# Performance work log

Hardware: AMD Instinct MI355X
Metric: run time of the kernel (lower is better)

Reference implementation:

```python
import jax, jax.numpy as jnp
import numpy as np

N_ACTIVE = 200000
K = 9  # filter_size [1,3,3] -> 9 kernel offsets
C = 64
EPS = 1e-5

def setup_inputs() -> dict:
    key = jax.random.key(0)
    ks = jax.random.split(key, 4)
    features = jax.random.normal(ks[0], (N_ACTIVE, C), dtype=jnp.float32)
    # rulebook: neighbor index per (active site, kernel offset); N_ACTIVE is the
    # sentinel meaning 'no active neighbor at this offset'
    nbr = jax.random.randint(ks[1], (N_ACTIVE, K), 0, N_ACTIVE + 1, dtype=jnp.int32)
    # identity offset (center of 3x3) always maps to self, as in submanifold conv
    nbr = nbr.at[:, K // 2].set(jnp.arange(N_ACTIVE, dtype=jnp.int32))
    W1 = jax.random.normal(ks[2], (K, C, C), dtype=jnp.float32) * (2.0 / (K * C)) ** 0.5
    W2 = jax.random.normal(ks[3], (K, C, C), dtype=jnp.float32) * (2.0 / (K * C)) ** 0.5
    gamma1 = jnp.ones((C,), jnp.float32); beta1 = jnp.zeros((C,), jnp.float32)
    gamma2 = jnp.ones((C,), jnp.float32); beta2 = jnp.zeros((C,), jnp.float32)
    return {"features": features, "nbr": nbr, "W1": W1, "gamma1": gamma1,
            "beta1": beta1, "W2": W2, "gamma2": gamma2, "beta2": beta2}

def _subm_conv(x, nbr, W):
    # gather-GEMM(-scatter) submanifold conv over active voxels
    xp = jnp.concatenate([x, jnp.zeros((1, x.shape[1]), x.dtype)], axis=0)  # zero row for sentinel
    g = xp[nbr]  # [N, K, Cin] irregular gather
    return jnp.einsum('nkc,kcd->nd', g, W)

def _bn(x, gamma, beta):
    mu = jnp.mean(x, axis=0)
    var = jnp.var(x, axis=0)
    return (x - mu) * jax.lax.rsqrt(var + EPS) * gamma + beta

def reference(features, nbr, W1, gamma1, beta1, W2, gamma2, beta2):
    out = _subm_conv(features, nbr, W1)
    out = jax.nn.relu(_bn(out, gamma1, beta1))   # scn.BatchNormReLU
    out = _subm_conv(out, nbr, W2)
    out = _bn(out, gamma2, beta2)                # scn.BatchNormalization
    return out + features                        # scn.AddTable with Identity residual
```

## Files before the change

### kernel.cpp

```cpp
#include <hip/hip_runtime.h>
#include <hip/hip_bf16.h>

#define NS 200000
#define KF 9
#define CC 64
#define RPB 128
#define NB ((NS + RPB - 1) / RPB)

typedef __bf16 bf16_t;
typedef __bf16 bf16x8 __attribute__((ext_vector_type(8)));
typedef __bf16 bf16x4 __attribute__((ext_vector_type(4)));
typedef float f32x4 __attribute__((ext_vector_type(4)));

__global__ void k_prep(const float* __restrict__ x, const float* __restrict__ W1,
                       const float* __restrict__ W2, bf16_t* __restrict__ xb,
                       bf16_t* __restrict__ W1p, bf16_t* __restrict__ W2p,
                       float* __restrict__ stats , float* __restrict__ zrow ) {
  const int b = blockIdx.x;
  const int tid = threadIdx.x;
  if (b < 12500) {
    if (b == 0) {
      stats[tid] = 0.f;
      if (tid < 32) zrow[tid] = 0.f;
    }
    long base = ((long)b * 256 + tid) * 4;
    const float4 v = *(const float4*)(x + base);
    bf16x4 o;
    o[0] = (bf16_t)v.x; o[1] = (bf16_t)v.y; o[2] = (bf16_t)v.z; o[3] = (bf16_t)v.w;
    *(bf16x4*)(xb + base) = o;
    return;
  }
  int b2 = b - 12500;
  const float* W = (b2 < 144) ? W1 : W2;
  bf16_t* Wp = (b2 < 144) ? W1p : W2p;
  if (b2 >= 144) b2 -= 144;
  int p = b2 * 256 + tid;
  int j = p & 7;
  int lane = (p >> 3) & 63;
  int kstep = (p >> 9) & 1;
  int ntile = (p >> 10) & 3;
  int k = p >> 12;
  int col = ntile * 16 + (lane & 15);
  int kk = kstep * 32 + 8 * (lane >> 4) + j;
  Wp[p] = (bf16_t)W[(k * CC + kk) * CC + col];
}

template <int OUT_F32>
__global__ __launch_bounds__(256, 3) void k_conv(
    const bf16_t* __restrict__ xb,
    const int* __restrict__ nbr,
    const bf16_t* __restrict__ Wp,
    void* __restrict__ yv,
    float* __restrict__ stats,
    const char* __restrict__ zrow)
{
  __shared__ int nbr_s[RPB * KF];
  __shared__ float lred[8 * CC];

  const int tid = threadIdx.x;
  const int lane = tid & 63;
  const int wid = tid >> 6;
  const int row0 = blockIdx.x * RPB;
  const int l15 = lane & 15;
  const int lhi = lane >> 4;

  {
    const long nbase = (long)row0 * KF;
    const long ntot = (long)NS * KF;
#pragma unroll
    for (int t = 0; t < 5; ++t) {
      int p = tid + t * 256;
      if (p < RPB * KF) {
        long g = nbase + p;
        nbr_s[p] = (g < ntot) ? nbr[g] : NS;
      }
    }
  }
  __syncthreads();

  const char* xbb = (const char*)xb;
  const bf16x8* wp = (const bf16x8*)Wp;
  const int r_lo = (32 * wid + l15) * KF;
  const int r_hi = (32 * wid + 16 + l15) * KF;

  auto rowptr = [&](int u) -> const char* {
    return ((unsigned)u < NS) ? (xbb + (size_t)(unsigned)u * 128u) : zrow;
  };

  int id0[KF], id1[KF];
#pragma unroll
  for (int k = 0; k < KF; ++k) { id0[k] = nbr_s[r_lo + k]; id1[k] = nbr_s[r_hi + k]; }

  f32x4 acc[2][4];
#pragma unroll
  for (int m = 0; m < 2; ++m)
#pragma unroll
    for (int n = 0; n < 4; ++n) acc[m][n] = (f32x4){0.f, 0.f, 0.f, 0.f};

  bf16x8 Af[4][2][2];
  bf16x8 cB[4][2], nB[4][2];

  auto loadA = [&](int slot, int k) {
    const char* s0 = rowptr(id0[k]);
    const char* s1 = rowptr(id1[k]);
    Af[slot][0][0] = *(const bf16x8*)(s0 + lhi * 16);
    Af[slot][0][1] = *(const bf16x8*)(s0 + 64 + lhi * 16);
    Af[slot][1][0] = *(const bf16x8*)(s1 + lhi * 16);
    Af[slot][1][1] = *(const bf16x8*)(s1 + 64 + lhi * 16);
  };

#pragma unroll
  for (int n = 0; n < 4; ++n)
#pragma unroll
    for (int kk = 0; kk < 2; ++kk)
      cB[n][kk] = wp[((0 * 4 + n) * 2 + kk) * 64 + lane];
#pragma unroll
  for (int k = 0; k < 3; ++k) loadA(k, k);

#pragma unroll
  for (int k = 0; k < KF; ++k) {
    if (k + 3 < KF) loadA((k + 3) & 3, k + 3);
    if (k + 1 < KF) {
#pragma unroll
      for (int n = 0; n < 4; ++n)
#pragma unroll
        for (int kk = 0; kk < 2; ++kk)
          nB[n][kk] = wp[(((k + 1) * 4 + n) * 2 + kk) * 64 + lane];
    }
    const int sl = k & 3;
    __builtin_amdgcn_s_setprio(1);
#pragma unroll
    for (int m = 0; m < 2; ++m)
#pragma unroll
      for (int n = 0; n < 4; ++n)
        acc[m][n] = __builtin_amdgcn_mfma_f32_16x16x32_bf16(Af[sl][m][0], cB[n][0], acc[m][n], 0, 0, 0);
#pragma unroll
    for (int m = 0; m < 2; ++m)
#pragma unroll
      for (int n = 0; n < 4; ++n)
        acc[m][n] = __builtin_amdgcn_mfma_f32_16x16x32_bf16(Af[sl][m][1], cB[n][1], acc[m][n], 0, 0, 0);
    __builtin_amdgcn_s_setprio(0);
#pragma unroll
    for (int n = 0; n < 4; ++n) { cB[n][0] = nB[n][0]; cB[n][1] = nB[n][1]; }
  }

  float csum[4] = {0.f, 0.f, 0.f, 0.f}, csq[4] = {0.f, 0.f, 0.f, 0.f};
  bf16_t* yb = (bf16_t*)yv;
  float* yf = (float*)yv;
#pragma unroll
  for (int m = 0; m < 2; ++m) {
    const int rb0 = row0 + 32 * wid + 16 * m + 4 * lhi;
#pragma unroll
    for (int n = 0; n < 4; ++n) {
      const int col = 16 * n + l15;
#pragma unroll
      for (int j = 0; j < 4; ++j) {
        float v = acc[m][n][j];
        csum[n] += v; csq[n] += v * v;
        int rb = rb0 + j;
        if (rb < NS) {
          if (OUT_F32) yf[(long)rb * CC + col] = v;
          else         yb[(long)rb * CC + col] = (bf16_t)v;
        }
      }
    }
  }
#pragma unroll
  for (int n = 0; n < 4; ++n) {
    csum[n] += __shfl_xor(csum[n], 16); csum[n] += __shfl_xor(csum[n], 32);
    csq[n]  += __shfl_xor(csq[n], 16);  csq[n]  += __shfl_xor(csq[n], 32);
  }
  if (lane < 16) {
#pragma unroll
    for (int n = 0; n < 4; ++n) {
      lred[wid * CC + 16 * n + l15] = csum[n];
      lred[4 * CC + wid * CC + 16 * n + l15] = csq[n];
    }
  }
  __syncthreads();
  if (tid < CC) {
    float s = lred[tid] + lred[CC + tid] + lred[2 * CC + tid] + lred[3 * CC + tid];
    float q = lred[4 * CC + tid] + lred[5 * CC + tid] + lred[6 * CC + tid] + lred[7 * CC + tid];
    atomicAdd(&stats[tid], s);
    atomicAdd(&stats[64 + tid], q);
  }
}

__global__ void k_bnrelu(const bf16_t* __restrict__ in, const float* __restrict__ stats,
                         const float* __restrict__ gamma, const float* __restrict__ beta,
                         bf16_t* __restrict__ out) {
  __shared__ float ss_s[128];
  const int tid = threadIdx.x;
  if (tid < 64) {
    const float invN = 1.0f / (float)NS;
    float mean = stats[tid] * invN;
    float var = fmaxf(stats[64 + tid] * invN - mean * mean, 0.f);
    float rs = rsqrtf(var + 1e-5f);
    float sc = gamma[tid] * rs;
    ss_s[tid] = sc;
    ss_s[64 + tid] = beta[tid] - mean * sc;
  }
  __syncthreads();
  long base = ((long)blockIdx.x * 256 + tid) * 8;
  bf16x8 v = *(const bf16x8*)(in + base);
  int c0 = (int)(base & 63);
  bf16x8 o;
#pragma unroll
  for (int j = 0; j < 8; ++j) {
    float f = (float)v[j] * ss_s[c0 + j] + ss_s[64 + c0 + j];
    o[j] = (bf16_t)fmaxf(f, 0.f);
  }
  *(bf16x8*)(out + base) = o;
}

__global__ void k_final(float* __restrict__ io, const float* __restrict__ stats,
                        const float* __restrict__ gamma, const float* __restrict__ beta,
                        const float* __restrict__ x) {
  __shared__ float ss_s[128];
  const int tid = threadIdx.x;
  if (tid < 64) {
    const float invN = 1.0f / (float)NS;
    float mean = stats[tid] * invN;
    float var = fmaxf(stats[64 + tid] * invN - mean * mean, 0.f);
    float rs = rsqrtf(var + 1e-5f);
    float sc = gamma[tid] * rs;
    ss_s[tid] = sc;
    ss_s[64 + tid] = beta[tid] - mean * sc;
  }
  __syncthreads();
  long base = ((long)blockIdx.x * 256 + tid) * 4;
  float4 v = *(const float4*)(io + base);
  float4 f = *(const float4*)(x + base);
  int c0 = (int)(base & 63);
  v.x = v.x * ss_s[c0 + 0] + ss_s[64 + c0 + 0] + f.x;
  v.y = v.y * ss_s[c0 + 1] + ss_s[64 + c0 + 1] + f.y;
  v.z = v.z * ss_s[c0 + 2] + ss_s[64 + c0 + 2] + f.z;
  v.w = v.w * ss_s[c0 + 3] + ss_s[64 + c0 + 3] + f.w;
  *(float4*)(io + base) = v;
}

extern "C" void kernel_launch(void* const* d_in, const int* in_sizes, int n_in,
                              void* d_out, int out_size, void* d_ws, size_t ws_size,
                              hipStream_t stream) {
  const float* features = (const float*)d_in[0];
  const int* nbr        = (const int*)d_in[1];
  const float* W1       = (const float*)d_in[2];
  const float* gamma1   = (const float*)d_in[3];
  const float* beta1    = (const float*)d_in[4];
  const float* W2       = (const float*)d_in[5];
  const float* gamma2   = (const float*)d_in[6];
  const float* beta2    = (const float*)d_in[7];

  bf16_t* xb  = (bf16_t*)d_out;
  bf16_t* o1  = (bf16_t*)((char*)d_out + (size_t)NS * CC * 2);
  float*  o2f = (float*)d_out;

  char* ws = (char*)d_ws;
  auto alignup = [](size_t x) { return (x + 255) & ~(size_t)255; };
  size_t off = 0;
  bf16_t* y1n = (bf16_t*)(ws + off); off += alignup((size_t)NS * CC * 2);
  bf16_t* W1p = (bf16_t*)(ws + off); off += alignup((size_t)KF * 4096 * 2);
  bf16_t* W2p = (bf16_t*)(ws + off); off += alignup((size_t)KF * 4096 * 2);
  float* stats = (float*)(ws + off); off += alignup(256 * 4);
  float* zrow  = (float*)(ws + off); off += alignup(32 * 4);

  k_prep<<<12500 + 288, 256, 0, stream>>>(features, W1, W2, xb, W1p, W2p, stats, zrow);

  k_conv<0><<<NB, 256, 0, stream>>>(xb, nbr, W1p, (void*)o1, stats, (const char*)zrow);
  k_bnrelu<<<6250, 256, 0, stream>>>(o1, stats, gamma1, beta1, y1n);

  k_conv<1><<<NB, 256, 0, stream>>>(y1n, nbr, W2p, (void*)o2f, stats + 128, (const char*)zrow);
  k_final<<<12500, 256, 0, stream>>>(o2f, stats + 128, gamma2, beta2, features);
}
```

Baseline: 283.7 us.

## Fuse BN+ReLU into second conv gather and stage rows via LDS async loads

Removes the separate BN-ReLU pass by applying the scale, shift and ReLU to gathered neighbor rows inside the second conv, masking the shift for sentinel rows. Gathered rows now go through a swizzled three-slot LDS ring using global_load_lds with explicit vmcnt waits, instead of being loaded straight into registers. Rows per block drop to 64, with one MFMA row tile per wave and an occupancy hint of 4. The second conv writes bf16 and the final kernel reads it, which cuts intermediate traffic at some precision cost. The scale and shift are stored in bf16, and the bounds checks now rely on NS being divisible by 64.

```diff
diff --git a/kernel.cpp b/kernel.cpp
--- a/kernel.cpp
+++ b/kernel.cpp
@@ -4,8 +4,8 @@
 #define NS 200000
 #define KF 9
 #define CC 64
-#define RPB 128
-#define NB ((NS + RPB - 1) / RPB)
+#define RPB 64
+#define NB (NS / RPB)
 
 typedef __bf16 bf16_t;
 typedef __bf16 bf16x8 __attribute__((ext_vector_type(8)));
@@ -45,17 +45,21 @@
   Wp[p] = (bf16_t)W[(k * CC + kk) * CC + col];
 }
 
-template <int OUT_F32>
-__global__ __launch_bounds__(256, 3) void k_conv(
-    const bf16_t* __restrict__ xb,
+template <int FUSE_BN>
+__global__ __launch_bounds__(256, 4) void k_conv(
+    const bf16_t* __restrict__ xsrc,
     const int* __restrict__ nbr,
     const bf16_t* __restrict__ Wp,
-    void* __restrict__ yv,
-    float* __restrict__ stats,
+    bf16_t* __restrict__ y,
+    float* __restrict__ stats_out,
+    const float* __restrict__ stats_in,
+    const float* __restrict__ gamma, const float* __restrict__ beta,
     const char* __restrict__ zrow)
 {
+  __shared__ __align__(16) char Aring[4 * 3 * 2048];
   __shared__ int nbr_s[RPB * KF];
   __shared__ float lred[8 * CC];
+  __shared__ __align__(16) bf16_t ssb[128];
 
   const int tid = threadIdx.x;
   const int lane = tid & 63;
@@ -65,61 +69,67 @@
   const int lhi = lane >> 4;
 
   {
-    const long nbase = (long)row0 * KF;
-    const long ntot = (long)NS * KF;
-#pragma unroll
-    for (int t = 0; t < 5; ++t) {
-      int p = tid + t * 256;
-      if (p < RPB * KF) {
-        long g = nbase + p;
-        nbr_s[p] = (g < ntot) ? nbr[g] : NS;
-      }
+    const int* src = nbr + (long)row0 * KF;
+    nbr_s[tid] = src[tid];
+    nbr_s[tid + 256] = src[tid + 256];
+    if (tid < 64) nbr_s[tid + 512] = src[tid + 512];
+  }
+  if (FUSE_BN) {
+    if (tid < 64) {
+      const float invN = 1.0f / (float)NS;
+      float mean = stats_in[tid] * invN;
+      float var = fmaxf(stats_in[64 + tid] * invN - mean * mean, 0.f);
+      float rs = rsqrtf(var + 1e-5f);
+      float sc = gamma[tid] * rs;
+      ssb[tid] = (bf16_t)sc;
+      ssb[64 + tid] = (bf16_t)(beta[tid] - mean * sc);
     }
   }
   __syncthreads();
 
-  const char* xbb = (const char*)xb;
+  const char* xbb = (const char*)xsrc;
+  char* ringw = Aring + wid * 6144;
+  const int sgrp = lane >> 3;
+  const int schunk = (lane & 7) ^ sgrp;
+
+  auto stageA = [&](int s, int k) {
+#pragma unroll
+    for (int i = 0; i < 2; ++i) {
+      int rloc = 8 * i + sgrp;
+      unsigned u = (unsigned)nbr_s[(16 * wid + rloc) * KF + k];
+      const char* gp = (u < NS) ? (xbb + (size_t)u * 128u + schunk * 16)
+                                : (zrow + schunk * 16);
+      __builtin_amdgcn_global_load_lds(
+          (const __attribute__((address_space(1))) void*)gp,
+          (__attribute__((address_space(3))) void*)(ringw + s * 2048 + i * 1024),
+          16, 0, 0);
+    }
+  };
+
   const bf16x8* wp = (const bf16x8*)Wp;
-  const int r_lo = (32 * wid + l15) * KF;
-  const int r_hi = (32 * wid + 16 + l15) * KF;
-
-  auto rowptr = [&](int u) -> const char* {
-    return ((unsigned)u < NS) ? (xbb + (size_t)(unsigned)u * 128u) : zrow;
-  };
-
-  int id0[KF], id1[KF];
-#pragma unroll
-  for (int k = 0; k < KF; ++k) { id0[k] = nbr_s[r_lo + k]; id1[k] = nbr_s[r_hi + k]; }
-
-  f32x4 acc[2][4];
-#pragma unroll
-  for (int m = 0; m < 2; ++m)
-#pragma unroll
-    for (int n = 0; n < 4; ++n) acc[m][n] = (f32x4){0.f, 0.f, 0.f, 0.f};
-
-  bf16x8 Af[4][2][2];
+  f32x4 acc[4];
+#pragma unroll
+  for (int n = 0; n < 4; ++n) acc[n] = (f32x4){0.f, 0.f, 0.f, 0.f};
+
   bf16x8 cB[4][2], nB[4][2];
-
-  auto loadA = [&](int slot, int k) {
-    const char* s0 = rowptr(id0[k]);
-    const char* s1 = rowptr(id1[k]);
-    Af[slot][0][0] = *(const bf16x8*)(s0 + lhi * 16);
-    Af[slot][0][1] = *(const bf16x8*)(s0 + 64 + lhi * 16);
-    Af[slot][1][0] = *(const bf16x8*)(s1 + lhi * 16);
-    Af[slot][1][1] = *(const bf16x8*)(s1 + 64 + lhi * 16);
-  };
-
+  bf16x8 scb0, shb0, scb1, shb1;
+  if (FUSE_BN) {
+    scb0 = *(const bf16x8*)&ssb[8 * lhi];
+    shb0 = *(const bf16x8*)&ssb[64 + 8 * lhi];
+    scb1 = *(const bf16x8*)&ssb[32 + 8 * lhi];
+    shb1 = *(const bf16x8*)&ssb[96 + 8 * lhi];
+  }
+
+  stageA(0, 0);
+  stageA(1, 1);
 #pragma unroll
   for (int n = 0; n < 4; ++n)
 #pragma unroll
     for (int kk = 0; kk < 2; ++kk)
       cB[n][kk] = wp[((0 * 4 + n) * 2 + kk) * 64 + lane];
-#pragma unroll
-  for (int k = 0; k < 3; ++k) loadA(k, k);
 
 #pragma unroll
   for (int k = 0; k < KF; ++k) {
-    if (k + 3 < KF) loadA((k + 3) & 3, k + 3);
     if (k + 1 < KF) {
 #pragma unroll
       for (int n = 0; n < 4; ++n)
@@ -127,42 +137,47 @@
         for (int kk = 0; kk < 2; ++kk)
           nB[n][kk] = wp[(((k + 1) * 4 + n) * 2 + kk) * 64 + lane];
     }
-    const int sl = k & 3;
+    if (k + 2 < KF) stageA((k + 2) % 3, k + 2);
+    if (k < KF - 2)       asm volatile("s_waitcnt vmcnt(4)" ::: "memory");
+    else if (k == KF - 2) asm volatile("s_waitcnt vmcnt(2)" ::: "memory");
+    else                  asm volatile("s_waitcnt vmcnt(0)" ::: "memory");
+    __builtin_amdgcn_sched_barrier(0);
+
+    const char* sb = ringw + (k % 3) * 2048;
+    bf16x8 a0 = *(const bf16x8*)(sb + l15 * 128 + ((lhi ^ (l15 & 7)) * 16));
+    bf16x8 a1 = *(const bf16x8*)(sb + l15 * 128 + (((4 + lhi) ^ (l15 & 7)) * 16));
+    if (FUSE_BN) {
+      float vm = ((unsigned)nbr_s[(16 * wid + l15) * KF + k] < NS) ? 1.f : 0.f;
+#pragma unroll
+      for (int j = 0; j < 8; ++j) {
+        float f0 = (float)a0[j] * (float)scb0[j] + (float)shb0[j] * vm;
+        a0[j] = (bf16_t)fmaxf(f0, 0.f);
+        float f1 = (float)a1[j] * (float)scb1[j] + (float)shb1[j] * vm;
+        a1[j] = (bf16_t)fmaxf(f1, 0.f);
+      }
+    }
     __builtin_amdgcn_s_setprio(1);
 #pragma unroll
-    for (int m = 0; m < 2; ++m)
-#pragma unroll
-      for (int n = 0; n < 4; ++n)
-        acc[m][n] = __builtin_amdgcn_mfma_f32_16x16x32_bf16(Af[sl][m][0], cB[n][0], acc[m][n], 0, 0, 0);
-#pragma unroll
-    for (int m = 0; m < 2; ++m)
-#pragma unroll
-      for (int n = 0; n < 4; ++n)
-        acc[m][n] = __builtin_amdgcn_mfma_f32_16x16x32_bf16(Af[sl][m][1], cB[n][1], acc[m][n], 0, 0, 0);
+    for (int n = 0; n < 4; ++n)
+      acc[n] = __builtin_amdgcn_mfma_f32_16x16x32_bf16(a0, cB[n][0], acc[n], 0, 0, 0);
+#pragma unroll
+    for (int n = 0; n < 4; ++n)
+      acc[n] = __builtin_amdgcn_mfma_f32_16x16x32_bf16(a1, cB[n][1], acc[n], 0, 0, 0);
     __builtin_amdgcn_s_setprio(0);
 #pragma unroll
     for (int n = 0; n < 4; ++n) { cB[n][0] = nB[n][0]; cB[n][1] = nB[n][1]; }
   }
 
   float csum[4] = {0.f, 0.f, 0.f, 0.f}, csq[4] = {0.f, 0.f, 0.f, 0.f};
-  bf16_t* yb = (bf16_t*)yv;
-  float* yf = (float*)yv;
-#pragma unroll
-  for (int m = 0; m < 2; ++m) {
-    const int rb0 = row0 + 32 * wid + 16 * m + 4 * lhi;
-#pragma unroll
-    for (int n = 0; n < 4; ++n) {
-      const int col = 16 * n + l15;
-#pragma unroll
-      for (int j = 0; j < 4; ++j) {
-        float v = acc[m][n][j];
-        csum[n] += v; csq[n] += v * v;
-        int rb = rb0 + j;
-        if (rb < NS) {
-          if (OUT_F32) yf[(long)rb * CC + col] = v;
-          else         yb[(long)rb * CC + col] = (bf16_t)v;
-        }
-      }
+  const int rb0 = row0 + 16 * wid + 4 * lhi;
+#pragma unroll
+  for (int n = 0; n < 4; ++n) {
+    const int col = 16 * n + l15;
+#pragma unroll
+    for (int j = 0; j < 4; ++j) {
+      float v = acc[n][j];
+      csum[n] += v; csq[n] += v * v;
+      y[(long)(rb0 + j) * CC + col] = (bf16_t)v;
     }
   }
 #pragma unroll
@@ -181,14 +196,14 @@
   if (tid < CC) {
     float s = lred[tid] + lred[CC + tid] + lred[2 * CC + tid] + lred[3 * CC + tid];
     float q = lred[4 * CC + tid] + lred[5 * CC + tid] + lred[6 * CC + tid] + lred[7 * CC + tid];
-    atomicAdd(&stats[tid], s);
-    atomicAdd(&stats[64 + tid], q);
-  }
-}
-
-__global__ void k_bnrelu(const bf16_t* __restrict__ in, const float* __restrict__ stats,
-                         const float* __restrict__ gamma, const float* __restrict__ beta,
-                         bf16_t* __restrict__ out) {
+    atomicAdd(&stats_out[tid], s);
+    atomicAdd(&stats_out[64 + tid], q);
+  }
+}
+
+__global__ void k_final(const bf16_t* __restrict__ o2b, const float* __restrict__ stats,
+                        const float* __restrict__ gamma, const float* __restrict__ beta,
+                        const float* __restrict__ x, float* __restrict__ out) {
   __shared__ float ss_s[128];
   const int tid = threadIdx.x;
   if (tid < 64) {
@@ -201,42 +216,16 @@
     ss_s[64 + tid] = beta[tid] - mean * sc;
   }
   __syncthreads();
-  long base = ((long)blockIdx.x * 256 + tid) * 8;
-  bf16x8 v = *(const bf16x8*)(in + base);
-  int c0 = (int)(base & 63);
-  bf16x8 o;
-#pragma unroll
-  for (int j = 0; j < 8; ++j) {
-    float f = (float)v[j] * ss_s[c0 + j] + ss_s[64 + c0 + j];
-    o[j] = (bf16_t)fmaxf(f, 0.f);
-  }
-  *(bf16x8*)(out + base) = o;
-}
-
-__global__ void k_final(float* __restrict__ io, const float* __restrict__ stats,
-                        const float* __restrict__ gamma, const float* __restrict__ beta,
-                        const float* __restrict__ x) {
-  __shared__ float ss_s[128];
-  const int tid = threadIdx.x;
-  if (tid < 64) {
-    const float invN = 1.0f / (float)NS;
-    float mean = stats[tid] * invN;
-    float var = fmaxf(stats[64 + tid] * invN - mean * mean, 0.f);
-    float rs = rsqrtf(var + 1e-5f);
-    float sc = gamma[tid] * rs;
-    ss_s[tid] = sc;
-    ss_s[64 + tid] = beta[tid] - mean * sc;
-  }
-  __syncthreads();
   long base = ((long)blockIdx.x * 256 + tid) * 4;
-  float4 v = *(const float4*)(io + base);
+  bf16x4 v = *(const bf16x4*)(o2b + base);
   float4 f = *(const float4*)(x + base);
   int c0 = (int)(base & 63);
-  v.x = v.x * ss_s[c0 + 0] + ss_s[64 + c0 + 0] + f.x;
-  v.y = v.y * ss_s[c0 + 1] + ss_s[64 + c0 + 1] + f.y;
-  v.z = v.z * ss_s[c0 + 2] + ss_s[64 + c0 + 2] + f.z;
-  v.w = v.w * ss_s[c0 + 3] + ss_s[64 + c0 + 3] + f.w;
-  *(float4*)(io + base) = v;
+  float4 r;
+  r.x = (float)v[0] * ss_s[c0 + 0] + ss_s[64 + c0 + 0] + f.x;
+  r.y = (float)v[1] * ss_s[c0 + 1] + ss_s[64 + c0 + 1] + f.y;
+  r.z = (float)v[2] * ss_s[c0 + 2] + ss_s[64 + c0 + 2] + f.z;
+  r.w = (float)v[3] * ss_s[c0 + 3] + ss_s[64 + c0 + 3] + f.w;
+  *(float4*)(out + base) = r;
 }
 
 extern "C" void kernel_launch(void* const* d_in, const int* in_sizes, int n_in,
@@ -251,14 +240,13 @@
   const float* gamma2   = (const float*)d_in[6];
   const float* beta2    = (const float*)d_in[7];
 
-  bf16_t* xb  = (bf16_t*)d_out;
-  bf16_t* o1  = (bf16_t*)((char*)d_out + (size_t)NS * CC * 2);
-  float*  o2f = (float*)d_out;
+  bf16_t* xb = (bf16_t*)d_out;
+  bf16_t* o1 = (bf16_t*)((char*)d_out + (size_t)NS * CC * 2);
 
   char* ws = (char*)d_ws;
   auto alignup = [](size_t x) { return (x + 255) & ~(size_t)255; };
   size_t off = 0;
-  bf16_t* y1n = (bf16_t*)(ws + off); off += alignup((size_t)NS * CC * 2);
+  bf16_t* o2b = (bf16_t*)(ws + off); off += alignup((size_t)NS * CC * 2);
   bf16_t* W1p = (bf16_t*)(ws + off); off += alignup((size_t)KF * 4096 * 2);
   bf16_t* W2p = (bf16_t*)(ws + off); off += alignup((size_t)KF * 4096 * 2);
   float* stats = (float*)(ws + off); off += alignup(256 * 4);
@@ -266,9 +254,9 @@
 
   k_prep<<<12500 + 288, 256, 0, stream>>>(features, W1, W2, xb, W1p, W2p, stats, zrow);
 
-  k_conv<0><<<NB, 256, 0, stream>>>(xb, nbr, W1p, (void*)o1, stats, (const char*)zrow);
-  k_bnrelu<<<6250, 256, 0, stream>>>(o1, stats, gamma1, beta1, y1n);
-
-  k_conv<1><<<NB, 256, 0, stream>>>(y1n, nbr, W2p, (void*)o2f, stats + 128, (const char*)zrow);
-  k_final<<<12500, 256, 0, stream>>>(o2f, stats + 128, gamma2, beta2, features);
-}
+  k_conv<0><<<NB, 256, 0, stream>>>(xb, nbr, W1p, o1, stats,
+                                    stats, gamma1, beta1, (const char*)zrow);
+  k_conv<1><<<NB, 256, 0, stream>>>(o1, nbr, W2p, o2b, stats + 128,
+                                    stats, gamma1, beta1, (const char*)zrow);
+  k_final<<<12500, 256, 0, stream>>>(o2b, stats + 128, gamma2, beta2, features, (float*)d_out);
+}
```

Result: slower. 410.8 us (+44.8%).
